# Optimization experiments

Hardware: AMD Instinct MI355X
Metric: run time of the kernel (lower is better)

Reference implementation:

```python
import jax, jax.numpy as jnp
import numpy as np

C = 512
N_HEADS = 8
K_CH = C // N_HEADS          # 64
ROPE_D = int(K_CH * 0.5)     # 32, only first half of head dim is rotated
ROPE_BASE = 10000


def apply_rope(x):
    # x: [b, h, t, k_ch]; rotate first ROPE_D features, pass the rest through.
    t = x.shape[2]
    d = ROPE_D
    theta = 1.0 / (ROPE_BASE ** (jnp.arange(0, d, 2, dtype=jnp.float32) / d))  # [d/2]
    idx_theta = jnp.arange(t, dtype=jnp.float32)[:, None] * theta[None, :]     # [t, d/2]
    angles = jnp.concatenate([idx_theta, idx_theta], axis=-1)                  # [t, d]
    cos = jnp.cos(angles)[None, None, :, :].astype(x.dtype)
    sin = jnp.sin(angles)[None, None, :, :].astype(x.dtype)
    x_rope, x_pass = x[..., :d], x[..., d:]
    d2 = d // 2
    neg_half = jnp.concatenate([-x_rope[..., d2:], x_rope[..., :d2]], axis=-1)
    x_rope = x_rope * cos + neg_half * sin
    return jnp.concatenate([x_rope, x_pass], axis=-1)


def setup_inputs() -> dict:
    key = jax.random.key(0)
    ks = jax.random.split(key, 9)
    B, T = 16, 1024
    scale = 1.0 / np.sqrt(C)
    return {
        "x": jax.random.normal(ks[0], (B, C, T), dtype=jnp.float32),
        "Wq": jax.random.normal(ks[1], (C, C), dtype=jnp.float32) * scale,
        "bq": jax.random.normal(ks[2], (C,), dtype=jnp.float32) * 0.01,
        "Wk": jax.random.normal(ks[3], (C, C), dtype=jnp.float32) * scale,
        "bk": jax.random.normal(ks[4], (C,), dtype=jnp.float32) * 0.01,
        "Wv": jax.random.normal(ks[5], (C, C), dtype=jnp.float32) * scale,
        "bv": jax.random.normal(ks[6], (C,), dtype=jnp.float32) * 0.01,
        "Wo": jax.random.normal(ks[7], (C, C), dtype=jnp.float32) * scale,
        "bo": jax.random.normal(ks[8], (C,), dtype=jnp.float32) * 0.01,
    }


def reference(x, Wq, bq, Wk, bk, Wv, bv, Wo, bo):
    b, c, t = x.shape
    # 1x1 conv == channel matmul: [o,c] x [b,c,t] -> [b,o,t]
    q = jnp.einsum('oc,bct->bot', Wq, x) + bq[None, :, None]
    k = jnp.einsum('oc,bct->bot', Wk, x) + bk[None, :, None]
    v = jnp.einsum('oc,bct->bot', Wv, x) + bv[None, :, None]

    def to_heads(z):  # [b, c, t] -> [b, h, t, k_ch]
        return z.reshape(b, N_HEADS, K_CH, t).transpose(0, 1, 3, 2)

    q = apply_rope(to_heads(q))
    k = apply_rope(to_heads(k))
    v = to_heads(v)

    # scaled dot product attention (scale = 1/sqrt(head_dim))
    scores = jnp.einsum('bhqd,bhkd->bhqk', q, k) / np.sqrt(K_CH).astype(np.float32)
    attn = jax.nn.softmax(scores, axis=-1)
    out = jnp.einsum('bhqk,bhkd->bhqd', attn, v)  # [b, h, t, k_ch]

    out = out.transpose(0, 1, 3, 2).reshape(b, c, t)  # [b, c, t]
    return jnp.einsum('oc,bct->bot', Wo, out) + bo[None, :, None]
```

## Files before the change

kernel.cpp:

```cpp
#include <hip/hip_runtime.h>
#include <cmath>

#define B_  16
#define T_  1024
#define C_  512
#define NH_ 8
#define HD_ 64

#define AS1 __attribute__((address_space(1)))
#define AS3 __attribute__((address_space(3)))

#define FENCE_VM()   asm volatile("s_waitcnt vmcnt(0)" ::: "memory")
#define FENCE_LGKM() asm volatile("s_waitcnt lgkmcnt(0)" ::: "memory")

typedef __bf16 bf16_t;
typedef __bf16 bf16x8 __attribute__((ext_vector_type(8)));
typedef __bf16 bf16x4 __attribute__((ext_vector_type(4)));
typedef short  shortx8 __attribute__((ext_vector_type(8)));
typedef short  shortx4 __attribute__((ext_vector_type(4)));
typedef float  floatx4 __attribute__((ext_vector_type(4)));
typedef float  float4v __attribute__((ext_vector_type(4)));

__device__ inline float fast_exp2(float x) {
#if __has_builtin(__builtin_amdgcn_exp2f)
  return __builtin_amdgcn_exp2f(x);
#else
  float r; asm("v_exp_f32 %0, %1" : "=v"(r) : "v"(x)); return r;
#endif
}
__device__ inline float hw_sin_rev(float rev) {
  float r; asm("v_sin_f32 %0, %1" : "=v"(r) : "v"(rev)); return r;
}
__device__ inline float hw_cos_rev(float rev) {
  float r; asm("v_cos_f32 %0, %1" : "=v"(r) : "v"(rev)); return r;
}

template <typename V8>
__device__ inline auto mfma_impl(V8 a, V8 b, floatx4 c, int)
    -> decltype(__builtin_amdgcn_mfma_f32_16x16x32_bf16(a, b, c, 0, 0, 0)) {
  return __builtin_amdgcn_mfma_f32_16x16x32_bf16(a, b, c, 0, 0, 0);
}
template <typename V8>
__device__ inline floatx4 mfma_impl(V8 a, V8 b, floatx4 c, long) {
  return __builtin_amdgcn_mfma_f32_16x16x32_bf16(
      __builtin_bit_cast(shortx8, a), __builtin_bit_cast(shortx8, b), c, 0, 0, 0);
}
__device__ inline floatx4 mfma_bf16(bf16x8 a, bf16x8 b, floatx4 c) {
  return mfma_impl(a, b, c, 0);
}

__device__ inline floatx4 mfma16_bf16(bf16x4 a, bf16x4 b, floatx4 c) {
#if __has_builtin(__builtin_amdgcn_mfma_f32_16x16x16bf16_1k)
  return __builtin_amdgcn_mfma_f32_16x16x16bf16_1k(
      __builtin_bit_cast(shortx4, a), __builtin_bit_cast(shortx4, b), c, 0, 0, 0);
#else
  floatx4 d;
  asm("v_mfma_f32_16x16x16_bf16 %0, %1, %2, %3"
      : "=v"(d) : "v"(a), "v"(b), "0"(c));
  return d;
#endif
}

__global__ void prep(const float* __restrict__ x, bf16_t* __restrict__ xt,
                     const float* __restrict__ w0, const float* __restrict__ w1,
                     const float* __restrict__ w2, const float* __restrict__ w3,
                     bf16_t* __restrict__ d0, bf16_t* __restrict__ d1,
                     bf16_t* __restrict__ d2, bf16_t* __restrict__ d3) {
  const int tx = threadIdx.x, ty = threadIdx.y;
  if (blockIdx.z < 16) {
    __shared__ float tile[32][33];
    const int b = blockIdx.z;
    const int t0 = blockIdx.x * 32, c0 = blockIdx.y * 32;
    for (int i = ty; i < 32; i += 8)
      tile[i][tx] = x[((size_t)b * C_ + c0 + i) * T_ + t0 + tx];
    __syncthreads();
    for (int i = ty; i < 32; i += 8)
      xt[((size_t)b * T_ + t0 + i) * C_ + c0 + tx] = (bf16_t)tile[tx][i];
  } else {
    const float* s[4] = {w0, w1, w2, w3};
    bf16_t* d[4] = {d0, d1, d2, d3};
    const int tid = ty * 32 + tx;
    const int idx = (blockIdx.y * 32 + blockIdx.x) * 256 + tid;
    const int e0 = idx * 8;
    const int which = e0 >> 18;
    const int off = e0 & 262143;
    const float4v f0 = *(const float4v*)(s[which] + off);
    const float4v f1 = *(const float4v*)(s[which] + off + 4);
    bf16x8 o;
#pragma unroll
    for (int e = 0; e < 4; e++) { o[e] = (bf16_t)f0[e]; o[4 + e] = (bf16_t)f1[e]; }
    *(bf16x8*)(d[which] + off) = o;
  }
}

__global__ __launch_bounds__(256) void qkv_gemm(
    const bf16_t* __restrict__ Wq, const bf16_t* __restrict__ Wk, const bf16_t* __restrict__ Wv,
    const float* __restrict__ bq, const float* __restrict__ bk, const float* __restrict__ bv,
    const bf16_t* __restrict__ xt,
    bf16_t* __restrict__ qo, bf16_t* __restrict__ ko, bf16_t* __restrict__ vo) {
  const int which = blockIdx.z % 3;
  const int b = blockIdx.z / 3;
  const bf16_t* W = which == 0 ? Wq : (which == 1 ? Wk : Wv);
  const float* bias = which == 0 ? bq : (which == 1 ? bk : bv);
  const int wave = threadIdx.x >> 6, lane = threadIdx.x & 63;
  const int col = lane & 15, quad = lane >> 4;
  const int MbB = blockIdx.y * 128, NbB = blockIdx.x * 128;
  const int Mw = (wave >> 1) * 64, Nw = (wave & 1) * 64;
  const bf16_t* xb = xt + (size_t)b * T_ * C_;

  __shared__ bf16_t As[3][128 * 32];
  __shared__ bf16_t Bs[3][128 * 32];

  auto stageKV = [&](int i) {
    const int k0 = i * 32, buf = i % 3;
#pragma unroll
    for (int c = 0; c < 2; c++) {
      const int j = wave * 128 + c * 64 + lane;
      __builtin_amdgcn_global_load_lds(
          (const AS1 void*)(W + (MbB + (j >> 2)) * C_ + k0 + (j & 3) * 8),
          (AS3 void*)((char*)&As[buf][0] + wave * 2048 + c * 1024), 16, 0, 0);
    }
#pragma unroll
    for (int c = 0; c < 2; c++) {
      const int j = wave * 128 + c * 64 + lane;
      __builtin_amdgcn_global_load_lds(
          (const AS1 void*)(xb + (NbB + (j >> 2)) * C_ + k0 + (j & 3) * 8),
          (AS3 void*)((char*)&Bs[buf][0] + wave * 2048 + c * 1024), 16, 0, 0);
    }
  };

  floatx4 acc[4][4] = {};
  stageKV(0);
  stageKV(1);
  asm volatile("s_waitcnt vmcnt(4)\ns_barrier" ::: "memory");
  for (int i = 0; i < 16; i++) {
    if (i + 2 < 16) stageKV(i + 2);
    const bf16_t* a = &As[i % 3][0];
    const bf16_t* bb = &Bs[i % 3][0];
    bf16x8 af[4], bfr[4];
#pragma unroll
    for (int mi = 0; mi < 4; mi++)
      af[mi] = *(const bf16x8*)(a + (Mw + mi * 16 + col) * 32 + quad * 8);
#pragma unroll
    for (int ni = 0; ni < 4; ni++)
      bfr[ni] = *(const bf16x8*)(bb + (Nw + ni * 16 + col) * 32 + quad * 8);
#pragma unroll
    for (int mi = 0; mi < 4; mi++)
#pragma unroll
      for (int ni = 0; ni < 4; ni++)
        acc[mi][ni] = mfma_bf16(af[mi], bfr[ni], acc[mi][ni]);
    if (i < 14) {
      asm volatile("s_waitcnt vmcnt(4)\ns_barrier" ::: "memory");
    } else if (i == 14) {
      asm volatile("s_waitcnt vmcnt(0)\ns_barrier" ::: "memory");
    }
  }

  const int Mb = MbB + Mw, Nb = NbB + Nw;
#pragma unroll
  for (int mi = 0; mi < 4; mi++)
#pragma unroll
    for (int r = 0; r < 4; r++) {
      const float bval = bias[Mb + mi * 16 + quad * 4 + r];
#pragma unroll
      for (int ni = 0; ni < 4; ni++) acc[mi][ni][r] += bval;
    }

  const int h = Mb >> 6;
  if (which < 2) {
#pragma unroll
    for (int ni = 0; ni < 4; ni++) {
      const int t = Nb + ni * 16 + col;
#pragma unroll
      for (int r = 0; r < 4; r++) {
        const int dd = quad * 4 + r;
        const float theta_rev =
            fast_exp2(-(float)dd * 0.83048202372184059f - 2.6514961294723187f);
        float rev = (float)t * theta_rev;
        rev = rev - floorf(rev);
        const float sn = hw_sin_rev(rev), cs = hw_cos_rev(rev);
        const float a0 = acc[0][ni][r], a1 = acc[1][ni][r];
        acc[0][ni][r] = a0 * cs - a1 * sn;
        acc[1][ni][r] = a1 * cs + a0 * sn;
      }
    }
    bf16_t* out = which == 0 ? qo : ko;
#pragma unroll
    for (int mi = 0; mi < 4; mi++) {
      const int d0 = mi * 16 + quad * 4;
#pragma unroll
      for (int ni = 0; ni < 4; ni++) {
        const int t = Nb + ni * 16 + col;
        bf16x4 pk;
#pragma unroll
        for (int r = 0; r < 4; r++) pk[r] = (bf16_t)acc[mi][ni][r];
        *(bf16x4*)(out + ((size_t)(b * NH_ + h) * T_ + t) * HD_ + d0) = pk;
      }
    }
  } else {
#pragma unroll
    for (int mi = 0; mi < 4; mi++)
#pragma unroll
      for (int ni = 0; ni < 4; ni++) {
        const int t = Nb + ni * 16 + col;
#pragma unroll
        for (int r = 0; r < 4; r++) {
          const int d = mi * 16 + quad * 4 + r;
          vo[((size_t)(b * NH_ + h) * HD_ + d) * T_ + t] = (bf16_t)acc[mi][ni][r];
        }
      }
  }
}

__global__ __launch_bounds__(512, 4) void attn_kernel(
    const bf16_t* __restrict__ qb, const bf16_t* __restrict__ kb,
    const bf16_t* __restrict__ vtb, bf16_t* __restrict__ ob) {
  const int id = blockIdx.x;
  const int bh = id & 127;
  const int qt = id >> 7;
  const int tid = threadIdx.x;
  const int wave = tid >> 6, lane = tid & 63;
  const int col = lane & 15, quad = lane >> 4;
  const int tq0 = qt * 256 + wave * 32;

  const bf16_t* Q = qb + (size_t)bh * T_ * HD_;
  const bf16_t* K = kb + (size_t)bh * T_ * HD_;
  const bf16_t* VT = vtb + (size_t)bh * HD_ * T_;

  __shared__ bf16_t kvs[2][2][4096];

  auto stage = [&](const char* gRowBase, int rowStrideB, bf16_t* dst) {
    const int r = tid >> 3, ck = tid & 7;
    const char* src = gRowBase + r * rowStrideB + ((ck ^ (r & 7)) << 4);
    __builtin_amdgcn_global_load_lds(
        (const AS1 void*)src,
        (AS3 void*)((char*)dst + wave * 1024), 16, 0, 0);
  };
  auto stageKV = [&](int tk0, int buf) {
    stage((const char*)(K + (size_t)tk0 * HD_), HD_ * 2, &kvs[buf][0][0]);
    stage((const char*)VT + (size_t)tk0 * 2, T_ * 2, &kvs[buf][1][0]);
  };
  auto frag = [&](const bf16_t* base, int R, int cg) -> bf16x8 {
    return *(const bf16x8*)(base + R * 64 + ((cg ^ (R & 7)) << 3));
  };

  floatx4 oacc[2][4] = {};
  floatx4 lacc4[2] = {};
  const float CEXP = 0.18033688011112042f;

  stageKV(0, 0);
  bf16x8 qf[2][2];
#pragma unroll
  for (int g = 0; g < 2; g++)
#pragma unroll
    for (int kk = 0; kk < 2; kk++) {
      bf16x8 raw = *(const bf16x8*)(Q + (tq0 + g * 16 + col) * HD_ + kk * 32 + quad * 8);
#pragma unroll
      for (int e = 0; e < 8; e++) qf[g][kk][e] = (bf16_t)((float)raw[e] * CEXP);
    }
  FENCE_VM();
  __syncthreads();

  for (int it = 0; it < 16; it++) {
    const int buf = it & 1;
    if (it + 1 < 16) stageKV((it + 1) * 64, buf ^ 1);
    const bf16_t* kt = &kvs[buf][0][0];
    const bf16_t* vt = &kvs[buf][1][0];

    floatx4 s[2][4] = {};
#pragma unroll
    for (int ni = 0; ni < 4; ni++)
#pragma unroll
      for (int kk = 0; kk < 2; kk++) {
        const bf16x8 kf = frag(kt, ni * 16 + col, kk * 4 + quad);
        s[0][ni] = mfma_bf16(kf, qf[0][kk], s[0][ni]);
        s[1][ni] = mfma_bf16(kf, qf[1][kk], s[1][ni]);
      }

    bf16x4 p4[2][4];
#pragma unroll
    for (int g = 0; g < 2; g++)
#pragma unroll
      for (int ni = 0; ni < 4; ni++)
#pragma unroll
        for (int r = 0; r < 4; r++) {
          const float pv = fast_exp2(s[g][ni][r]);
          lacc4[g][r] += pv;
          p4[g][ni][r] = (bf16_t)pv;
        }

#pragma unroll
    for (int nd = 0; nd < 4; nd++) {
      const int R = nd * 16 + col;
      bf16x4 v4[4];
#pragma unroll
      for (int ni = 0; ni < 4; ni++) {
        const int c8 = ni * 2 + (quad >> 1);
        v4[ni] = *(const bf16x4*)(vt + R * 64 + ((c8 ^ (R & 7)) << 3) + (quad & 1) * 4);
      }
#pragma unroll
      for (int ni = 0; ni < 4; ni++) {
        oacc[0][nd] = mfma16_bf16(p4[0][ni], v4[ni], oacc[0][nd]);
        oacc[1][nd] = mfma16_bf16(p4[1][ni], v4[ni], oacc[1][nd]);
      }
    }

    FENCE_VM();
    __syncthreads();
  }

  float lrow[2];
#pragma unroll
  for (int g = 0; g < 2; g++) {
    lrow[g] = lacc4[g][0] + lacc4[g][1] + lacc4[g][2] + lacc4[g][3];
    lrow[g] += __shfl_xor(lrow[g], 16, 64);
    lrow[g] += __shfl_xor(lrow[g], 32, 64);
  }
  float linv[2][4];
#pragma unroll
  for (int g = 0; g < 2; g++)
#pragma unroll
    for (int r = 0; r < 4; r++)
      linv[g][r] = 1.0f / __shfl(lrow[g], quad * 4 + r, 64);
#pragma unroll
  for (int g = 0; g < 2; g++)
#pragma unroll
    for (int nd = 0; nd < 4; nd++)
#pragma unroll
      for (int r = 0; r < 4; r++) {
        const float v = oacc[g][nd][r] * linv[g][r];
        ob[((size_t)bh * T_ + tq0 + g * 16 + quad * 4 + r) * HD_ + nd * 16 + col] = (bf16_t)v;
      }
}

__global__ __launch_bounds__(256) void out_gemm(
    const bf16_t* __restrict__ W, const float* __restrict__ bias,
    const bf16_t* __restrict__ ao, float* __restrict__ y) {
  const int b = blockIdx.z;
  const int wave = threadIdx.x >> 6, lane = threadIdx.x & 63;
  const int col = lane & 15, quad = lane >> 4;
  const int MbB = blockIdx.y * 128, NbB = blockIdx.x * 128;
  const int Mw = (wave >> 1) * 64, Nw = (wave & 1) * 64;
  const bf16_t* ab = ao + (size_t)b * NH_ * T_ * HD_;

  __shared__ bf16_t As[3][128 * 32];
  __shared__ bf16_t Bs[3][128 * 32];

  auto stageKV = [&](int i) {
    const int k0 = i * 32, buf = i % 3;
#pragma unroll
    for (int c = 0; c < 2; c++) {
      const int j = wave * 128 + c * 64 + lane;
      __builtin_amdgcn_global_load_lds(
          (const AS1 void*)(W + (MbB + (j >> 2)) * C_ + k0 + (j & 3) * 8),
          (AS3 void*)((char*)&As[buf][0] + wave * 2048 + c * 1024), 16, 0, 0);
    }
#pragma unroll
    for (int c = 0; c < 2; c++) {
      const int j = wave * 128 + c * 64 + lane;
      const int kg = k0 + (j & 3) * 8;
      __builtin_amdgcn_global_load_lds(
          (const AS1 void*)(ab + ((size_t)(kg >> 6) * T_ + NbB + (j >> 2)) * HD_ + (kg & 63)),
          (AS3 void*)((char*)&Bs[buf][0] + wave * 2048 + c * 1024), 16, 0, 0);
    }
  };

  floatx4 acc[4][4] = {};
  stageKV(0);
  stageKV(1);
  asm volatile("s_waitcnt vmcnt(4)\ns_barrier" ::: "memory");
  for (int i = 0; i < 16; i++) {
    if (i + 2 < 16) stageKV(i + 2);
    const bf16_t* a = &As[i % 3][0];
    const bf16_t* bb = &Bs[i % 3][0];
    bf16x8 af[4], bfr[4];
#pragma unroll
    for (int mi = 0; mi < 4; mi++)
      af[mi] = *(const bf16x8*)(a + (Mw + mi * 16 + col) * 32 + quad * 8);
#pragma unroll
    for (int ni = 0; ni < 4; ni++)
      bfr[ni] = *(const bf16x8*)(bb + (Nw + ni * 16 + col) * 32 + quad * 8);
#pragma unroll
    for (int mi = 0; mi < 4; mi++)
#pragma unroll
      for (int ni = 0; ni < 4; ni++)
        acc[mi][ni] = mfma_bf16(af[mi], bfr[ni], acc[mi][ni]);
    if (i < 14) {
      asm volatile("s_waitcnt vmcnt(4)\ns_barrier" ::: "memory");
    } else if (i == 14) {
      asm volatile("s_waitcnt vmcnt(0)\ns_barrier" ::: "memory");
    }
  }

  const int Mb = MbB + Mw, Nb = NbB + Nw;
#pragma unroll
  for (int mi = 0; mi < 4; mi++)
#pragma unroll
    for (int r = 0; r < 4; r++) {
      const int o = Mb + mi * 16 + quad * 4 + r;
      const float bval = bias[o];
#pragma unroll
      for (int ni = 0; ni < 4; ni++) {
        const int t = Nb + ni * 16 + col;
        y[((size_t)b * C_ + o) * T_ + t] = acc[mi][ni][r] + bval;
      }
    }
}

extern "C" void kernel_launch(void* const* d_in, const int* in_sizes, int n_in,
                              void* d_out, int out_size, void* d_ws, size_t ws_size,
                              hipStream_t stream) {
  const float* x  = (const float*)d_in[0];
  const float* Wq = (const float*)d_in[1];
  const float* bq = (const float*)d_in[2];
  const float* Wk = (const float*)d_in[3];
  const float* bk = (const float*)d_in[4];
  const float* Wv = (const float*)d_in[5];
  const float* bv = (const float*)d_in[6];
  const float* Wo = (const float*)d_in[7];
  const float* bo = (const float*)d_in[8];
  float* y = (float*)d_out;

  char* ws = (char*)d_ws;
  const size_t WB = (size_t)C_ * C_ * 2;
  const size_t XB = (size_t)B_ * T_ * C_ * 2;
  bf16_t* wqb = (bf16_t*)(ws + 0 * WB);
  bf16_t* wkb = (bf16_t*)(ws + 1 * WB);
  bf16_t* wvb = (bf16_t*)(ws + 2 * WB);
  bf16_t* wob = (bf16_t*)(ws + 3 * WB);
  bf16_t* xt  = (bf16_t*)(ws + 4 * WB);
  bf16_t* qb_ = (bf16_t*)(ws + 4 * WB + 1 * XB);
  bf16_t* kb_ = (bf16_t*)(ws + 4 * WB + 2 * XB);
  bf16_t* vtb = (bf16_t*)(ws + 4 * WB + 3 * XB);
  bf16_t* aob = xt;

  prep<<<dim3(T_ / 32, C_ / 32, B_ + 1), dim3(32, 8), 0, stream>>>(
      x, xt, Wq, Wk, Wv, Wo, wqb, wkb, wvb, wob);
  qkv_gemm<<<dim3(T_ / 128, C_ / 128, B_ * 3), dim3(256), 0, stream>>>(
      wqb, wkb, wvb, bq, bk, bv, xt, qb_, kb_, vtb);
  attn_kernel<<<dim3((T_ / 256) * B_ * NH_), dim3(512), 0, stream>>>(qb_, kb_, vtb, aob);
  out_gemm<<<dim3(T_ / 128, C_ / 128, B_), dim3(256), 0, stream>>>(wob, bo, aob, y);
}
```

Before: 205.9 us.

## Fuse Q/K/V projections per head into one GEMM tile sharing x loads

The QKV GEMM now assigns each block one head and computes Q, K and V for that head together, so each x tile is loaded from global memory once instead of three times. Each block holds a 3x64x32 weight tile and a 128x32 activation tile, and the pipeline drops from triple buffering with partial vmcnt waits to double buffering with a full wait and barrier every step. Waves now split the 64 head dims as 32 rows each, so only waves holding dims 0-31 apply RoPE. The grid shrinks from 1536 to 1024 blocks, and the simpler pipeline may expose more load latency.

```diff
diff --git a/kernel.cpp b/kernel.cpp
--- a/kernel.cpp
+++ b/kernel.cpp
@@ -98,118 +98,131 @@
     const float* __restrict__ bq, const float* __restrict__ bk, const float* __restrict__ bv,
     const bf16_t* __restrict__ xt,
     bf16_t* __restrict__ qo, bf16_t* __restrict__ ko, bf16_t* __restrict__ vo) {
-  const int which = blockIdx.z % 3;
-  const int b = blockIdx.z / 3;
-  const bf16_t* W = which == 0 ? Wq : (which == 1 ? Wk : Wv);
-  const float* bias = which == 0 ? bq : (which == 1 ? bk : bv);
+  const int b = blockIdx.z;
+  const int h = blockIdx.y;
   const int wave = threadIdx.x >> 6, lane = threadIdx.x & 63;
   const int col = lane & 15, quad = lane >> 4;
-  const int MbB = blockIdx.y * 128, NbB = blockIdx.x * 128;
-  const int Mw = (wave >> 1) * 64, Nw = (wave & 1) * 64;
+  const int NbB = blockIdx.x * 128;
+  const int Mw = (wave >> 1) * 32, Nw = (wave & 1) * 64;
+  const int MbG = h * 64;
   const bf16_t* xb = xt + (size_t)b * T_ * C_;
 
-  __shared__ bf16_t As[3][128 * 32];
-  __shared__ bf16_t Bs[3][128 * 32];
-
-  auto stageKV = [&](int i) {
-    const int k0 = i * 32, buf = i % 3;
-#pragma unroll
-    for (int c = 0; c < 2; c++) {
-      const int j = wave * 128 + c * 64 + lane;
+  __shared__ __align__(16) bf16_t As[2][3 * 64 * 32];
+  __shared__ __align__(16) bf16_t Bs[2][128 * 32];
+
+  auto stageT = [&](int i, int buf) {
+    const int k0 = i * 32;
+#pragma unroll
+    for (int c = 0; c < 3; c++) {
+      const int jb = wave * 3 + c;
+      const int w = jb >> 2;
+      const int j = jb * 64 + lane;
+      const int rem = j & 255;
+      const int row = rem >> 2, koff = (rem & 3) * 8;
+      const bf16_t* Wsel = w == 0 ? Wq : (w == 1 ? Wk : Wv);
       __builtin_amdgcn_global_load_lds(
-          (const AS1 void*)(W + (MbB + (j >> 2)) * C_ + k0 + (j & 3) * 8),
-          (AS3 void*)((char*)&As[buf][0] + wave * 2048 + c * 1024), 16, 0, 0);
+          (const AS1 void*)(Wsel + (MbG + row) * C_ + k0 + koff),
+          (AS3 void*)((char*)&As[buf][0] + j * 16), 16, 0, 0);
     }
 #pragma unroll
     for (int c = 0; c < 2; c++) {
       const int j = wave * 128 + c * 64 + lane;
       __builtin_amdgcn_global_load_lds(
           (const AS1 void*)(xb + (NbB + (j >> 2)) * C_ + k0 + (j & 3) * 8),
-          (AS3 void*)((char*)&Bs[buf][0] + wave * 2048 + c * 1024), 16, 0, 0);
+          (AS3 void*)((char*)&Bs[buf][0] + j * 16), 16, 0, 0);
     }
   };
 
-  floatx4 acc[4][4] = {};
-  stageKV(0);
-  stageKV(1);
-  asm volatile("s_waitcnt vmcnt(4)\ns_barrier" ::: "memory");
+  floatx4 acc[3][2][4] = {};
+  stageT(0, 0);
+  FENCE_VM();
+  __syncthreads();
   for (int i = 0; i < 16; i++) {
-    if (i + 2 < 16) stageKV(i + 2);
-    const bf16_t* a = &As[i % 3][0];
-    const bf16_t* bb = &Bs[i % 3][0];
-    bf16x8 af[4], bfr[4];
-#pragma unroll
-    for (int mi = 0; mi < 4; mi++)
-      af[mi] = *(const bf16x8*)(a + (Mw + mi * 16 + col) * 32 + quad * 8);
+    const int buf = i & 1;
+    if (i + 1 < 16) stageT(i + 1, buf ^ 1);
+    const bf16_t* a = &As[buf][0];
+    const bf16_t* bb = &Bs[buf][0];
+    bf16x8 af[3][2], bfr[4];
+#pragma unroll
+    for (int w = 0; w < 3; w++)
+#pragma unroll
+      for (int mi = 0; mi < 2; mi++)
+        af[w][mi] = *(const bf16x8*)(a + w * 2048 + (Mw + mi * 16 + col) * 32 + quad * 8);
 #pragma unroll
     for (int ni = 0; ni < 4; ni++)
       bfr[ni] = *(const bf16x8*)(bb + (Nw + ni * 16 + col) * 32 + quad * 8);
 #pragma unroll
-    for (int mi = 0; mi < 4; mi++)
-#pragma unroll
-      for (int ni = 0; ni < 4; ni++)
-        acc[mi][ni] = mfma_bf16(af[mi], bfr[ni], acc[mi][ni]);
-    if (i < 14) {
-      asm volatile("s_waitcnt vmcnt(4)\ns_barrier" ::: "memory");
-    } else if (i == 14) {
-      asm volatile("s_waitcnt vmcnt(0)\ns_barrier" ::: "memory");
-    }
-  }
-
-  const int Mb = MbB + Mw, Nb = NbB + Nw;
-#pragma unroll
-  for (int mi = 0; mi < 4; mi++)
-#pragma unroll
-    for (int r = 0; r < 4; r++) {
-      const float bval = bias[Mb + mi * 16 + quad * 4 + r];
-#pragma unroll
-      for (int ni = 0; ni < 4; ni++) acc[mi][ni][r] += bval;
-    }
-
-  const int h = Mb >> 6;
-  if (which < 2) {
+    for (int w = 0; w < 3; w++)
+#pragma unroll
+      for (int mi = 0; mi < 2; mi++)
+#pragma unroll
+        for (int ni = 0; ni < 4; ni++)
+          acc[w][mi][ni] = mfma_bf16(af[w][mi], bfr[ni], acc[w][mi][ni]);
+    FENCE_VM();
+    __syncthreads();
+  }
+
+#pragma unroll
+  for (int w = 0; w < 3; w++) {
+    const float* bias = w == 0 ? bq : (w == 1 ? bk : bv);
+#pragma unroll
+    for (int mi = 0; mi < 2; mi++)
+#pragma unroll
+      for (int r = 0; r < 4; r++) {
+        const float bval = bias[MbG + Mw + mi * 16 + quad * 4 + r];
+#pragma unroll
+        for (int ni = 0; ni < 4; ni++) acc[w][mi][ni][r] += bval;
+      }
+  }
+
+  if (Mw == 0) {
+#pragma unroll
+    for (int w = 0; w < 2; w++)
+#pragma unroll
+      for (int ni = 0; ni < 4; ni++) {
+        const int t = NbB + Nw + ni * 16 + col;
+#pragma unroll
+        for (int r = 0; r < 4; r++) {
+          const int dd = quad * 4 + r;
+          const float theta_rev =
+              fast_exp2(-(float)dd * 0.83048202372184059f - 2.6514961294723187f);
+          float rev = (float)t * theta_rev;
+          rev = rev - floorf(rev);
+          const float sn = hw_sin_rev(rev), cs = hw_cos_rev(rev);
+          const float a0 = acc[w][0][ni][r], a1 = acc[w][1][ni][r];
+          acc[w][0][ni][r] = a0 * cs - a1 * sn;
+          acc[w][1][ni][r] = a1 * cs + a0 * sn;
+        }
+      }
+  }
+
+#pragma unroll
+  for (int w = 0; w < 2; w++) {
+    bf16_t* out = w == 0 ? qo : ko;
+#pragma unroll
+    for (int mi = 0; mi < 2; mi++) {
+      const int d0 = Mw + mi * 16 + quad * 4;
+#pragma unroll
+      for (int ni = 0; ni < 4; ni++) {
+        const int t = NbB + Nw + ni * 16 + col;
+        bf16x4 pk;
+#pragma unroll
+        for (int r = 0; r < 4; r++) pk[r] = (bf16_t)acc[w][mi][ni][r];
+        *(bf16x4*)(out + ((size_t)(b * NH_ + h) * T_ + t) * HD_ + d0) = pk;
+      }
+    }
+  }
+#pragma unroll
+  for (int mi = 0; mi < 2; mi++)
 #pragma unroll
     for (int ni = 0; ni < 4; ni++) {
-      const int t = Nb + ni * 16 + col;
+      const int t = NbB + Nw + ni * 16 + col;
 #pragma unroll
       for (int r = 0; r < 4; r++) {
-        const int dd = quad * 4 + r;
-        const float theta_rev =
-            fast_exp2(-(float)dd * 0.83048202372184059f - 2.6514961294723187f);
-        float rev = (float)t * theta_rev;
-        rev = rev - floorf(rev);
-        const float sn = hw_sin_rev(rev), cs = hw_cos_rev(rev);
-        const float a0 = acc[0][ni][r], a1 = acc[1][ni][r];
-        acc[0][ni][r] = a0 * cs - a1 * sn;
-        acc[1][ni][r] = a1 * cs + a0 * sn;
-      }
-    }
-    bf16_t* out = which == 0 ? qo : ko;
-#pragma unroll
-    for (int mi = 0; mi < 4; mi++) {
-      const int d0 = mi * 16 + quad * 4;
-#pragma unroll
-      for (int ni = 0; ni < 4; ni++) {
-        const int t = Nb + ni * 16 + col;
-        bf16x4 pk;
-#pragma unroll
-        for (int r = 0; r < 4; r++) pk[r] = (bf16_t)acc[mi][ni][r];
-        *(bf16x4*)(out + ((size_t)(b * NH_ + h) * T_ + t) * HD_ + d0) = pk;
-      }
-    }
-  } else {
-#pragma unroll
-    for (int mi = 0; mi < 4; mi++)
-#pragma unroll
-      for (int ni = 0; ni < 4; ni++) {
-        const int t = Nb + ni * 16 + col;
-#pragma unroll
-        for (int r = 0; r < 4; r++) {
-          const int d = mi * 16 + quad * 4 + r;
-          vo[((size_t)(b * NH_ + h) * HD_ + d) * T_ + t] = (bf16_t)acc[mi][ni][r];
-        }
-      }
-  }
+        const int d = Mw + mi * 16 + quad * 4 + r;
+        vo[((size_t)(b * NH_ + h) * HD_ + d) * T_ + t] = (bf16_t)acc[2][mi][ni][r];
+      }
+    }
 }
 
 __global__ __launch_bounds__(512, 4) void attn_kernel(
@@ -436,7 +449,7 @@
 
   prep<<<dim3(T_ / 32, C_ / 32, B_ + 1), dim3(32, 8), 0, stream>>>(
       x, xt, Wq, Wk, Wv, Wo, wqb, wkb, wvb, wob);
-  qkv_gemm<<<dim3(T_ / 128, C_ / 128, B_ * 3), dim3(256), 0, stream>>>(
+  qkv_gemm<<<dim3(T_ / 128, NH_, B_), dim3(256), 0, stream>>>(
       wqb, wkb, wvb, bq, bk, bv, xt, qb_, kb_, vtb);
   attn_kernel<<<dim3((T_ / 256) * B_ * NH_), dim3(512), 0, stream>>>(qb_, kb_, vtb, aob);
   out_gemm<<<dim3(T_ / 128, C_ / 128, B_), dim3(256), 0, stream>>>(wob, bo, aob, y);
```

Result: slower. 284.3 us (+38.1%).
